# Optimization experiments

Measured on AMD Instinct MI355X. Metric: run time of the kernel, lower is better.

The kernel has to match this reference:

```python
import jax, jax.numpy as jnp
import numpy as np
from jax import lax

CHUNK = 64
EPS = 1e-5


def chunk_gla(q, k, v, g, chunk=CHUNK):
    """Gated linear attention, chunked parallel form (scale=1, as in HGRN2).
    q,k,g: [B,H,L,DK]; v: [B,H,L,DV]; g is per-step log decay on key dims.
    Recurrence: S_t = diag(exp(g_t)) S_{t-1} + k_t^T v_t ; o_t = q_t S_t.
    """
    B, H, L, DK = q.shape
    DV = v.shape[-1]
    n = L // chunk
    qc = q.reshape(B, H, n, chunk, DK)
    kc = k.reshape(B, H, n, chunk, DK)
    vc = v.reshape(B, H, n, chunk, DV)
    gc = jnp.cumsum(g.reshape(B, H, n, chunk, DK), axis=3)   # inclusive cumsum of log decays
    g_last = gc[..., -1:, :]                                 # [B,H,n,1,DK] total chunk decay

    qg = qc * jnp.exp(gc)                 # decay-weighted queries
    kg = kc * jnp.exp(g_last - gc)        # keys scaled to end-of-chunk
    kd = kc * jnp.exp(-gc)                # keys unscaled for intra-chunk attn

    # intra-chunk causal attention
    A = jnp.einsum('bhntd,bhnsd->bhnts', qg, kd)
    mask = jnp.tril(jnp.ones((chunk, chunk), dtype=bool))
    A = jnp.where(mask, A, 0.0)
    o_intra = jnp.einsum('bhnts,bhnsd->bhntd', A, vc)

    # inter-chunk recurrence over n chunks
    def step(S, inp):
        qg_c, kg_c, vc_c, gl_c = inp  # [B,H,C,DK], [B,H,C,DK], [B,H,C,DV], [B,H,DK]
        o = jnp.einsum('bhtd,bhdv->bhtv', qg_c, S)
        S = S * jnp.exp(gl_c)[..., None] + jnp.einsum('bhtd,bhtv->bhdv', kg_c, vc_c)
        return S, o

    S0 = jnp.zeros((B, H, DK, DV), q.dtype)
    xs = (jnp.moveaxis(qg, 2, 0), jnp.moveaxis(kg, 2, 0),
          jnp.moveaxis(vc, 2, 0), jnp.moveaxis(g_last[..., 0, :], 2, 0))
    _, o_inter = lax.scan(step, S0, xs)   # [n,B,H,C,DV]
    o = o_intra + jnp.moveaxis(o_inter, 0, 2)
    return o.reshape(B, H, L, DV)


def rms_norm(x, w, eps=EPS):
    var = jnp.mean(jnp.square(x), axis=-1, keepdims=True)
    return x * lax.rsqrt(var + eps) * w


def setup_inputs() -> dict:
    key = jax.random.key(0)
    B, L, D = 4, 2048, 2048
    ks = jax.random.split(key, 6)
    s = 1.0 / np.sqrt(D)
    return {
        'x': jax.random.normal(ks[0], (B, L, D), jnp.float32),
        'Wq': jax.random.normal(ks[1], (D, D), jnp.float32) * s,
        'Wf': jax.random.normal(ks[2], (D, D), jnp.float32) * s,
        'Wi': jax.random.normal(ks[3], (D, D), jnp.float32) * s,
        'Wo': jax.random.normal(ks[4], (D, D), jnp.float32) * s,
        'gnorm_w': jnp.ones((D,), jnp.float32),
    }


def reference(x, Wq, Wf, Wi, Wo, gnorm_w):
    B, L, D = x.shape
    H = 16
    Dh = D // H

    q = jax.nn.sigmoid(x @ Wq.T)
    f = jax.nn.sigmoid(x @ Wf.T)
    i = x @ Wi.T
    k = 1.0 - f
    g = jnp.log(f)

    def split_heads(t):  # b l (h d) -> b h l d
        return t.reshape(B, L, H, Dh).transpose(0, 2, 1, 3)

    q, k, i, g = map(split_heads, (q, k, i, g))
    o = chunk_gla(q, k, i, g)                  # [B,H,L,Dh]
    o = o.transpose(0, 2, 1, 3).reshape(B, L, D)
    o = rms_norm(o, gnorm_w)
    return o @ Wo.T
```

## Files before the change

kernel.cpp:

```cpp
#include <hip/hip_runtime.h>
#include <math.h>

typedef __bf16 bf16_t;
typedef __bf16 bf16x8 __attribute__((ext_vector_type(8)));
typedef float  f32x4  __attribute__((ext_vector_type(4)));

__device__ __forceinline__ void gl2lds16(const void* g, void* l) {
  __builtin_amdgcn_global_load_lds((__attribute__((address_space(1))) void*)g,
                                   (__attribute__((address_space(3))) void*)l,
                                   16, 0, 0);
}

#define MFMA16(a, b, c) __builtin_amdgcn_mfma_f32_16x16x32_bf16(a, b, c, 0, 0, 0)

template<int MODE>
__global__ __launch_bounds__(256, 2)
void gemm_bt2(const bf16_t* __restrict__ A, const bf16_t* __restrict__ Bw,
              bf16_t* __restrict__ oq, bf16_t* __restrict__ okk,
              bf16_t* __restrict__ ov, float* __restrict__ og,
              float* __restrict__ of, const float* __restrict__ rsc,
              int M, int N, int K)
{
  __shared__ __align__(16) bf16_t As[128 * 64];
  __shared__ __align__(16) bf16_t Bs[128 * 64];
  const int tt   = threadIdx.x;
  const int wave = tt >> 6;
  const int lane = tt & 63;
  const int nbn = N >> 7;
  const int m0 = (int)(blockIdx.x / nbn) << 7;
  const int n0 = (int)(blockIdx.x % nbn) << 7;
  const int wr = (wave >> 1) * 64;
  const int wc = (wave & 1) * 64;
  const int l15 = lane & 15, lq = lane >> 4;

  const int tk0 = (lq * 16) ^ ((lane & 7) << 4);
  const int tk1 = (64 + lq * 16) ^ ((lane & 7) << 4);

  const int srow = wave * 8 + (lane >> 3);
  const int sg = (lane & 7) ^ (lane >> 3);
  const bf16_t* pA = A  + (size_t)(m0 + srow) * K + sg * 8;
  const bf16_t* pB = Bw + (size_t)(n0 + srow) * K + sg * 8;

  f32x4 acc[4][4] = {};

  for (int kt = 0; kt < K; kt += 64) {
    #pragma unroll
    for (int i = 0; i < 4; i++) {
      gl2lds16(pA + (size_t)i * 32 * K + kt, (void*)(As + wave * 512 + i * 2048));
      gl2lds16(pB + (size_t)i * 32 * K + kt, (void*)(Bs + wave * 512 + i * 2048));
    }
    asm volatile("s_waitcnt vmcnt(0)" ::: "memory");
    __syncthreads();

    bf16x8 a[2][4], b[2][4];
    #pragma unroll
    for (int mf = 0; mf < 4; mf++) {
      const char* rp = (const char*)As + (wr + mf * 16 + l15) * 128;
      a[0][mf] = *(const bf16x8*)(rp + tk0);
      a[1][mf] = *(const bf16x8*)(rp + tk1);
    }
    #pragma unroll
    for (int nf = 0; nf < 4; nf++) {
      const char* rp = (const char*)Bs + (wc + nf * 16 + l15) * 128;
      b[0][nf] = *(const bf16x8*)(rp + tk0);
      b[1][nf] = *(const bf16x8*)(rp + tk1);
    }
    #pragma unroll
    for (int kh = 0; kh < 2; kh++)
      #pragma unroll
      for (int mf = 0; mf < 4; mf++)
        #pragma unroll
        for (int nf = 0; nf < 4; nf++)
          acc[mf][nf] = MFMA16(a[kh][mf], b[kh][nf], acc[mf][nf]);
    __syncthreads();
  }

  const int er = lq * 4;
  if (MODE == 0) {
    const int seg = n0 >> 11;
    const int gc = (n0 & 2047) + wc;
    #pragma unroll
    for (int mf = 0; mf < 4; mf++)
      #pragma unroll
      for (int nf = 0; nf < 4; nf++) {
        const int gr = m0 + wr + mf * 16 + er;
        #pragma unroll
        for (int jj = 0; jj < 4; jj++) {
          const size_t off2 = (size_t)(gr + jj) * 2048 + gc + nf * 16 + l15;
          const float v = acc[mf][nf][jj];
          if (seg == 0) {
            oq[off2] = (bf16_t)(1.0f / (1.0f + expf(-v)));
          } else if (seg == 1) {
            okk[off2] = (bf16_t)(1.0f / (1.0f + expf(v)));
            og[off2] = fminf(v, 0.0f) - log1pf(expf(-fabsf(v)));
          } else {
            ov[off2] = (bf16_t)v;
          }
        }
      }
  } else {
    const int gc = n0 + wc + l15;
    #pragma unroll
    for (int mf = 0; mf < 4; mf++) {
      const int gr = m0 + wr + mf * 16 + er;
      #pragma unroll
      for (int jj = 0; jj < 4; jj++) {
        const float s = rsc[gr + jj];
        #pragma unroll
        for (int nf = 0; nf < 4; nf++)
          of[(size_t)(gr + jj) * N + gc + nf * 16] = acc[mf][nf][jj] * s;
      }
    }
  }
}

__global__ void f2b_kernel(const float* __restrict__ in, bf16_t* __restrict__ out, int n8)
{
  const int idx = blockIdx.x * 256 + threadIdx.x;
  if (idx >= n8) return;
  const float4 a = *(const float4*)(in + (size_t)idx * 8);
  const float4 b = *(const float4*)(in + (size_t)idx * 8 + 4);
  bf16x8 o;
  o[0] = (bf16_t)a.x; o[1] = (bf16_t)a.y; o[2] = (bf16_t)a.z; o[3] = (bf16_t)a.w;
  o[4] = (bf16_t)b.x; o[5] = (bf16_t)b.y; o[6] = (bf16_t)b.z; o[7] = (bf16_t)b.w;
  *(bf16x8*)(out + (size_t)idx * 8) = o;
}

__global__ void f2b3_kernel(const float* __restrict__ w0, const float* __restrict__ w1,
                            const float* __restrict__ w2, bf16_t* __restrict__ out, int n8)
{
  const int idx = blockIdx.x * 256 + threadIdx.x;
  if (idx >= 3 * n8) return;
  const int which = idx / n8, j = idx - which * n8;
  const float* src = (which == 0) ? w0 : (which == 1) ? w1 : w2;
  const float4 a = *(const float4*)(src + (size_t)j * 8);
  const float4 b = *(const float4*)(src + (size_t)j * 8 + 4);
  bf16x8 o;
  o[0] = (bf16_t)a.x; o[1] = (bf16_t)a.y; o[2] = (bf16_t)a.z; o[3] = (bf16_t)a.w;
  o[4] = (bf16_t)b.x; o[5] = (bf16_t)b.y; o[6] = (bf16_t)b.z; o[7] = (bf16_t)b.w;
  *(bf16x8*)(out + (size_t)idx * 8) = o;
}

__global__ void f2bw_kernel(const float* __restrict__ in, const float* __restrict__ gw,
                            bf16_t* __restrict__ out, int n8)
{
  const int idx = blockIdx.x * 256 + threadIdx.x;
  if (idx >= n8) return;
  const int k0 = (idx * 8) & 2047;
  const float4 a = *(const float4*)(in + (size_t)idx * 8);
  const float4 b = *(const float4*)(in + (size_t)idx * 8 + 4);
  const float4 g0 = *(const float4*)(gw + k0);
  const float4 g1 = *(const float4*)(gw + k0 + 4);
  bf16x8 o;
  o[0] = (bf16_t)(a.x * g0.x); o[1] = (bf16_t)(a.y * g0.y);
  o[2] = (bf16_t)(a.z * g0.z); o[3] = (bf16_t)(a.w * g0.w);
  o[4] = (bf16_t)(b.x * g1.x); o[5] = (bf16_t)(b.y * g1.y);
  o[6] = (bf16_t)(b.z * g1.z); o[7] = (bf16_t)(b.w * g1.w);
  *(bf16x8*)(out + (size_t)idx * 8) = o;
}

__global__ __launch_bounds__(256)
void prep2_kernel(bf16_t* __restrict__ qb, bf16_t* __restrict__ kb,
                  const float* __restrict__ g32, float* __restrict__ eglh)
{
  __shared__ __align__(16) float gs[64][132];
  __shared__ float gls[128];
  const int blk = blockIdx.x;
  const int c = blk & 31, h = (blk >> 5) & 15, b = blk >> 9;
  const size_t row0 = (size_t)b * 2048 + (size_t)c * 64;
  const int col0 = h * 128;
  const int tt = threadIdx.x;

  #pragma unroll
  for (int s = 0; s < 8; s++) {
    const int u = tt + s * 256;
    const int t = u >> 5, d4 = (u & 31) * 4;
    *(float4*)&gs[t][d4] = *(const float4*)(g32 + (row0 + t) * 2048 + col0 + d4);
  }
  __syncthreads();
  if (tt < 128) {
    float run = 0.0f;
    for (int t = 0; t < 64; t++) { run += gs[t][tt]; gs[t][tt] = run; }
    gls[tt] = 0.5f * run;
    eglh[(size_t)blk * 128 + tt] = expf(0.5f * run);
  }
  __syncthreads();
  #pragma unroll
  for (int s = 0; s < 4; s++) {
    const int u = tt + s * 256;
    const int t = u >> 4, d8 = (u & 15) * 8;
    bf16_t* qp = qb + (row0 + t) * 2048 + col0 + d8;
    bf16_t* kp = kb + (row0 + t) * 2048 + col0 + d8;
    const bf16x8 q8 = *(const bf16x8*)qp;
    const bf16x8 k8 = *(const bf16x8*)kp;
    bf16x8 qo, ko2;
    #pragma unroll
    for (int j = 0; j < 8; j++) {
      const float gc = gs[t][d8 + j];
      const float gh = gls[d8 + j];
      qo[j]  = (bf16_t)((float)q8[j] * expf(gc - gh));
      ko2[j] = (bf16_t)((float)k8[j] * expf(gh - gc));
    }
    *(bf16x8*)qp = qo;
    *(bf16x8*)kp = ko2;
  }
}

__global__ __launch_bounds__(256)
void state2_kernel(const bf16_t* __restrict__ kb, const bf16_t* __restrict__ vb,
                   const float* __restrict__ eglh, bf16_t* __restrict__ ST)
{
  __shared__ __align__(16) bf16_t kgt[64][72];
  __shared__ __align__(16) bf16_t vt[64][72];
  __shared__ float ehs[64];
  const int blk = blockIdx.x;
  const int dh = blk & 1, eh = (blk >> 1) & 1, bh = blk >> 2;
  const int b = bh >> 4, h = bh & 15;
  const int col0 = h * 128;
  const int tt = threadIdx.x, wave = tt >> 6, lane = tt & 63;
  const int r = lane & 15, ko = (lane >> 4) * 8;
  const int d0 = dh * 64, e0 = eh * 64;
  f32x4 acc[4] = {};

  for (int c = 0; c < 32; c++) {
    const size_t cb = (size_t)bh * 32 + c;
    const size_t row0 = (size_t)b * 2048 + (size_t)c * 64;
    if (tt < 64) ehs[tt] = eglh[cb * 128 + d0 + tt];
    __syncthreads();
    #pragma unroll
    for (int s = 0; s < 2; s++) {
      const int u = tt + s * 256;
      const int t = u >> 3, d8 = (u & 7) * 8;
      const bf16x8 kv = *(const bf16x8*)(kb + (row0 + t) * 2048 + col0 + d0 + d8);
      const bf16x8 vv = *(const bf16x8*)(vb + (row0 + t) * 2048 + col0 + e0 + d8);
      #pragma unroll
      for (int j = 0; j < 8; j++) {
        kgt[d8 + j][t] = (bf16_t)((float)kv[j] * ehs[d8 + j]);
        vt[d8 + j][t]  = vv[j];
      }
    }
    __syncthreads();
    #pragma unroll
    for (int nf = 0; nf < 4; nf++) {
      const int d = nf * 16 + r;
      const float sd = ehs[d];
      #pragma unroll
      for (int jj = 0; jj < 4; jj++) {
        const int e = e0 + wave * 16 + (lane >> 4) * 4 + jj;
        ST[(cb * 128 + e) * 128 + d0 + d] = (bf16_t)(acc[nf][jj] * sd);
      }
    }
    #pragma unroll
    for (int nf = 0; nf < 4; nf++) {
      const float ev = ehs[nf * 16 + r];
      const float e2 = ev * ev;
      #pragma unroll
      for (int jj = 0; jj < 4; jj++) acc[nf][jj] *= e2;
    }
    #pragma unroll
    for (int ks = 0; ks < 2; ks++) {
      const bf16x8 a = *(const bf16x8*)&vt[wave * 16 + r][ks * 32 + ko];
      #pragma unroll
      for (int nf = 0; nf < 4; nf++) {
        const bf16x8 bfr = *(const bf16x8*)&kgt[nf * 16 + r][ks * 32 + ko];
        acc[nf] = MFMA16(a, bfr, acc[nf]);
      }
    }
    __syncthreads();
  }
}

__global__ __launch_bounds__(256)
void chunk2_kernel(const bf16_t* __restrict__ qb, const bf16_t* __restrict__ kb,
                   const bf16_t* __restrict__ vb, const bf16_t* __restrict__ ST,
                   bf16_t* __restrict__ o16)
{
  __shared__ __align__(16) bf16_t qgs[64][136];
  __shared__ __align__(16) bf16_t kds[64][136];
  __shared__ __align__(16) bf16_t vTs[128][72];
  __shared__ __align__(16) bf16_t Ps[64][72];
  const int blk = blockIdx.x;
  const int c = blk & 31, h = (blk >> 5) & 15, b = blk >> 9;
  const size_t row0 = (size_t)b * 2048 + (size_t)c * 64;
  const int col0 = h * 128;
  const int tt = threadIdx.x, wave = tt >> 6, lane = tt & 63;
  const int r = lane & 15, ko = (lane >> 4) * 8;

  #pragma unroll
  for (int s = 0; s < 4; s++) {
    const int u = tt + s * 256;
    const int t = u >> 4, d8 = (u & 15) * 8;
    *(bf16x8*)&qgs[t][d8] = *(const bf16x8*)(qb + (row0 + t) * 2048 + col0 + d8);
    *(bf16x8*)&kds[t][d8] = *(const bf16x8*)(kb + (row0 + t) * 2048 + col0 + d8);
  }
  #pragma unroll
  for (int s = 0; s < 4; s++) {
    const int u = tt + s * 256;
    const int t = u >> 4, e8 = (u & 15) * 8;
    const bf16x8 vv = *(const bf16x8*)(vb + (row0 + t) * 2048 + col0 + e8);
    #pragma unroll
    for (int j = 0; j < 8; j++) vTs[e8 + j][t] = vv[j];
  }
  __syncthreads();

  bf16x8 aq[4];
  #pragma unroll
  for (int ks = 0; ks < 4; ks++) aq[ks] = *(const bf16x8*)&qgs[wave * 16 + r][ks * 32 + ko];

  f32x4 accA[4] = {};
  #pragma unroll
  for (int ks = 0; ks < 4; ks++)
    #pragma unroll
    for (int sf = 0; sf < 4; sf++) {
      const bf16x8 bfr = *(const bf16x8*)&kds[sf * 16 + r][ks * 32 + ko];
      accA[sf] = MFMA16(aq[ks], bfr, accA[sf]);
    }

  #pragma unroll
  for (int sf = 0; sf < 4; sf++)
    #pragma unroll
    for (int jj = 0; jj < 4; jj++) {
      const int t = wave * 16 + (lane >> 4) * 4 + jj;
      const int s = sf * 16 + r;
      Ps[t][s] = (bf16_t)(t >= s ? accA[sf][jj] : 0.0f);
    }

  f32x4 acc[8] = {};
  const size_t stbase = (size_t)blk * 128 * 128;
  #pragma unroll
  for (int ks = 0; ks < 4; ks++)
    #pragma unroll
    for (int ne = 0; ne < 8; ne++) {
      const bf16x8 bfr = *(const bf16x8*)(ST + stbase + (size_t)(ne * 16 + r) * 128 + ks * 32 + ko);
      acc[ne] = MFMA16(aq[ks], bfr, acc[ne]);
    }
  #pragma unroll
  for (int ks = 0; ks < 2; ks++) {
    const bf16x8 pa = *(const bf16x8*)&Ps[wave * 16 + r][ks * 32 + ko];
    #pragma unroll
    for (int ne = 0; ne < 8; ne++) {
      const bf16x8 bfr = *(const bf16x8*)&vTs[ne * 16 + r][ks * 32 + ko];
      acc[ne] = MFMA16(pa, bfr, acc[ne]);
    }
  }

  #pragma unroll
  for (int ne = 0; ne < 8; ne++)
    #pragma unroll
    for (int jj = 0; jj < 4; jj++) {
      const int t = wave * 16 + (lane >> 4) * 4 + jj;
      const int e = ne * 16 + r;
      o16[(row0 + t) * 2048 + col0 + e] = (bf16_t)acc[ne][jj];
    }
}

__global__ __launch_bounds__(256)
void rmsr_kernel(const bf16_t* __restrict__ o16, float* __restrict__ rsc)
{
  __shared__ float red[4];
  const size_t row = blockIdx.x;
  const int tt = threadIdx.x;
  const bf16x8 v = *(const bf16x8*)(o16 + row * 2048 + tt * 8);
  float ss = 0.0f;
  #pragma unroll
  for (int j = 0; j < 8; j++) { const float f = (float)v[j]; ss += f * f; }
  #pragma unroll
  for (int off = 32; off > 0; off >>= 1) ss += __shfl_down(ss, off);
  if ((tt & 63) == 0) red[tt >> 6] = ss;
  __syncthreads();
  if (tt == 0)
    rsc[row] = rsqrtf((red[0] + red[1] + red[2] + red[3]) * (1.0f / 2048.0f) + 1e-5f);
}

extern "C" void kernel_launch(void* const* d_in, const int* in_sizes, int n_in,
                              void* d_out, int out_size, void* d_ws, size_t ws_size,
                              hipStream_t stream)
{
  const float* x  = (const float*)d_in[0];
  const float* Wq = (const float*)d_in[1];
  const float* Wf = (const float*)d_in[2];
  const float* Wi = (const float*)d_in[3];
  const float* Wo = (const float*)d_in[4];
  const float* gw = (const float*)d_in[5];
  float* out = (float*)d_out;
  char* ws = (char*)d_ws;

  const int K = 2048;
  const size_t MB = 1ull << 20;

  auto run = [&](const float* xs, float* outs, int nbs) {
    const int Ms = nbs * 2048;
    const size_t Sx = (size_t)Ms * 2048 * 2;
    bf16_t* xb  = (bf16_t*)(ws + 0);
    bf16_t* qb  = (bf16_t*)(ws + Sx);
    bf16_t* kb  = (bf16_t*)(ws + 2 * Sx);
    bf16_t* vb  = (bf16_t*)(ws + 3 * Sx);
    float*  g32 = (float*) (ws + 4 * Sx);
    bf16_t* Wb  = (bf16_t*)(ws + 6 * Sx);
    float*  egh = (float*) (ws + 6 * Sx + 24 * MB);
    float*  rsc = (float*) (ws + 6 * Sx + 25 * MB);
    bf16_t* STp = (bf16_t*)(ws + 4 * Sx);
    bf16_t* o16 = (bf16_t*)(ws + 0);

    const int n8x = Ms * 2048 / 8;
    const int n8w = 2048 * 2048 / 8;

    f2b_kernel<<<(n8x + 255) / 256, 256, 0, stream>>>(xs, xb, n8x);
    f2b3_kernel<<<(3 * n8w + 255) / 256, 256, 0, stream>>>(Wq, Wf, Wi, Wb, n8w);

    gemm_bt2<0><<<(Ms / 128) * (6144 / 128), 256, 0, stream>>>(
        xb, Wb, qb, kb, vb, g32, nullptr, nullptr, Ms, 6144, K);

    prep2_kernel<<<nbs * 512, 256, 0, stream>>>(qb, kb, g32, egh);
    state2_kernel<<<nbs * 64, 256, 0, stream>>>(kb, vb, egh, STp);
    chunk2_kernel<<<nbs * 512, 256, 0, stream>>>(qb, kb, vb, STp, o16);
    rmsr_kernel<<<Ms, 256, 0, stream>>>(o16, rsc);

    f2bw_kernel<<<(n8w + 255) / 256, 256, 0, stream>>>(Wo, gw, Wb, n8w);
    gemm_bt2<1><<<(Ms / 128) * (2048 / 128), 256, 0, stream>>>(
        o16, Wb, nullptr, nullptr, nullptr, nullptr, outs, rsc, Ms, 2048, K);
  };

  const size_t Sx_full = (size_t)8192 * 2048 * 2;
  const size_t need_full = 6 * Sx_full + 26 * MB;
  if (ws_size >= need_full) {
    run(x, out, 4);
  } else {
    for (int sb = 0; sb < 4; sb++)
      run(x + (size_t)sb * 2048 * 2048, out + (size_t)sb * 2048 * 2048, 1);
  }

  (void)in_sizes; (void)n_in; (void)out_size;
}
```

Baseline: 591.0 us.

## Use 256x256 double-buffered LDS GEMM for fused QKV projection

Replaces the 128x128 tile GEMM for the QKV projection (M=8192, N=6144) with a new 512-thread kernel using 256x256 tiles. Each k-step is staged into a second 64KB LDS buffer with async global-to-LDS loads while the current one is computed, so loads overlap with MFMA work. Larger tiles raise arithmetic intensity and cut global traffic. In exchange, 128KB of dynamic LDS and 128 accumulator registers per lane limit occupancy to one block per CU, and the grid shrinks to 768 blocks. The output projection keeps the old kernel, now specialised to that single mode.

```diff
diff --git a/kernel.cpp b/kernel.cpp
--- a/kernel.cpp
+++ b/kernel.cpp
@@ -13,11 +13,106 @@
 
 #define MFMA16(a, b, c) __builtin_amdgcn_mfma_f32_16x16x32_bf16(a, b, c, 0, 0, 0)
 
-template<int MODE>
+__global__ __launch_bounds__(512, 1)
+void gemm256s(const bf16_t* __restrict__ A, const bf16_t* __restrict__ Bw,
+              bf16_t* __restrict__ oq, bf16_t* __restrict__ okk,
+              bf16_t* __restrict__ ov, float* __restrict__ og,
+              int M, int N, int K)
+{
+  extern __shared__ __align__(16) char smem[];
+  const int tt = threadIdx.x;
+  const int wave = tt >> 6, lane = tt & 63;
+  const int wm = wave >> 2, wn = wave & 3;
+  const int nbn = N >> 8;
+  const int m0 = (int)(blockIdx.x / nbn) << 8;
+  const int n0 = (int)(blockIdx.x % nbn) << 8;
+  const int l15 = lane & 15, lq = lane >> 4;
+
+  const int tk0 = (lq * 16) ^ ((lane & 7) << 4);
+  const int tk1 = (64 + lq * 16) ^ ((lane & 7) << 4);
+
+  const int srow = tt >> 3;
+  const int sg = (tt & 7) ^ (srow & 7);
+  const bf16_t* pA = A  + (size_t)(m0 + srow) * K + sg * 8;
+  const bf16_t* pB = Bw + (size_t)(n0 + srow) * K + sg * 8;
+  const size_t rstep = (size_t)64 * K;
+
+  f32x4 acc[8][4] = {};
+  const int T = K >> 6;
+
+  auto stage = [&](int t, int sl) {
+    const int kt = t << 6;
+    char* base = smem + sl * 65536 + tt * 16;
+    #pragma unroll
+    for (int i = 0; i < 4; i++) {
+      gl2lds16(pA + i * rstep + kt, base + i * 8192);
+      gl2lds16(pB + i * rstep + kt, base + 32768 + i * 8192);
+    }
+  };
+
+  stage(0, 0);
+
+  for (int t = 0; t < T; t++) {
+    const int s = t & 1;
+    asm volatile("s_waitcnt vmcnt(0)" ::: "memory");
+    __builtin_amdgcn_s_barrier();
+    if (t + 1 < T) stage(t + 1, s ^ 1);
+
+    const char* as = smem + s * 65536;
+    const char* bs = as + 32768;
+
+    bf16x8 bfr[4][2];
+    #pragma unroll
+    for (int nf = 0; nf < 4; nf++) {
+      const char* rp = bs + (wn * 64 + nf * 16 + l15) * 128;
+      bfr[nf][0] = *(const bf16x8*)(rp + tk0);
+      bfr[nf][1] = *(const bf16x8*)(rp + tk1);
+    }
+    #pragma unroll
+    for (int h = 0; h < 2; h++) {
+      bf16x8 af[4][2];
+      #pragma unroll
+      for (int mf = 0; mf < 4; mf++) {
+        const char* rp = as + (wm * 128 + (h * 4 + mf) * 16 + l15) * 128;
+        af[mf][0] = *(const bf16x8*)(rp + tk0);
+        af[mf][1] = *(const bf16x8*)(rp + tk1);
+      }
+      #pragma unroll
+      for (int mf = 0; mf < 4; mf++)
+        #pragma unroll
+        for (int nf = 0; nf < 4; nf++) {
+          acc[h * 4 + mf][nf] = MFMA16(af[mf][0], bfr[nf][0], acc[h * 4 + mf][nf]);
+          acc[h * 4 + mf][nf] = MFMA16(af[mf][1], bfr[nf][1], acc[h * 4 + mf][nf]);
+        }
+    }
+  }
+
+  const int er = lq * 4;
+  const int seg = n0 >> 11;
+  const int gc = (n0 & 2047) + wn * 64 + l15;
+  #pragma unroll
+  for (int mf = 0; mf < 8; mf++)
+    #pragma unroll
+    for (int nf = 0; nf < 4; nf++) {
+      const int gr = m0 + wm * 128 + mf * 16 + er;
+      #pragma unroll
+      for (int jj = 0; jj < 4; jj++) {
+        const size_t off2 = (size_t)(gr + jj) * 2048 + gc + nf * 16;
+        const float v = acc[mf][nf][jj];
+        if (seg == 0) {
+          oq[off2] = (bf16_t)(1.0f / (1.0f + expf(-v)));
+        } else if (seg == 1) {
+          okk[off2] = (bf16_t)(1.0f / (1.0f + expf(v)));
+          og[off2] = fminf(v, 0.0f) - log1pf(expf(-fabsf(v)));
+        } else {
+          ov[off2] = (bf16_t)v;
+        }
+      }
+    }
+}
+
 __global__ __launch_bounds__(256, 2)
 void gemm_bt2(const bf16_t* __restrict__ A, const bf16_t* __restrict__ Bw,
-              bf16_t* __restrict__ oq, bf16_t* __restrict__ okk,
-              bf16_t* __restrict__ ov, float* __restrict__ og,
               float* __restrict__ of, const float* __restrict__ rsc,
               int M, int N, int K)
 {
@@ -76,40 +171,16 @@
   }
 
   const int er = lq * 4;
-  if (MODE == 0) {
-    const int seg = n0 >> 11;
-    const int gc = (n0 & 2047) + wc;
-    #pragma unroll
-    for (int mf = 0; mf < 4; mf++)
-      #pragma unroll
-      for (int nf = 0; nf < 4; nf++) {
-        const int gr = m0 + wr + mf * 16 + er;
-        #pragma unroll
-        for (int jj = 0; jj < 4; jj++) {
-          const size_t off2 = (size_t)(gr + jj) * 2048 + gc + nf * 16 + l15;
-          const float v = acc[mf][nf][jj];
-          if (seg == 0) {
-            oq[off2] = (bf16_t)(1.0f / (1.0f + expf(-v)));
-          } else if (seg == 1) {
-            okk[off2] = (bf16_t)(1.0f / (1.0f + expf(v)));
-            og[off2] = fminf(v, 0.0f) - log1pf(expf(-fabsf(v)));
-          } else {
-            ov[off2] = (bf16_t)v;
-          }
-        }
-      }
-  } else {
-    const int gc = n0 + wc + l15;
-    #pragma unroll
-    for (int mf = 0; mf < 4; mf++) {
-      const int gr = m0 + wr + mf * 16 + er;
-      #pragma unroll
-      for (int jj = 0; jj < 4; jj++) {
-        const float s = rsc[gr + jj];
-        #pragma unroll
-        for (int nf = 0; nf < 4; nf++)
-          of[(size_t)(gr + jj) * N + gc + nf * 16] = acc[mf][nf][jj] * s;
-      }
+  const int gc = n0 + wc + l15;
+  #pragma unroll
+  for (int mf = 0; mf < 4; mf++) {
+    const int gr = m0 + wr + mf * 16 + er;
+    #pragma unroll
+    for (int jj = 0; jj < 4; jj++) {
+      const float s = rsc[gr + jj];
+      #pragma unroll
+      for (int nf = 0; nf < 4; nf++)
+        of[(size_t)(gr + jj) * N + gc + nf * 16] = acc[mf][nf][jj] * s;
     }
   }
 }
@@ -387,6 +458,10 @@
 
   const int K = 2048;
   const size_t MB = 1ull << 20;
+  const int LDS = 131072;
+
+  (void)hipFuncSetAttribute((const void*)gemm256s,
+      hipFuncAttributeMaxDynamicSharedMemorySize, LDS);
 
   auto run = [&](const float* xs, float* outs, int nbs) {
     const int Ms = nbs * 2048;
@@ -408,8 +483,8 @@
     f2b_kernel<<<(n8x + 255) / 256, 256, 0, stream>>>(xs, xb, n8x);
     f2b3_kernel<<<(3 * n8w + 255) / 256, 256, 0, stream>>>(Wq, Wf, Wi, Wb, n8w);
 
-    gemm_bt2<0><<<(Ms / 128) * (6144 / 128), 256, 0, stream>>>(
-        xb, Wb, qb, kb, vb, g32, nullptr, nullptr, Ms, 6144, K);
+    gemm256s<<<(Ms / 256) * (6144 / 256), 512, LDS, stream>>>(
+        xb, Wb, qb, kb, vb, g32, Ms, 6144, K);
 
     prep2_kernel<<<nbs * 512, 256, 0, stream>>>(qb, kb, g32, egh);
     state2_kernel<<<nbs * 64, 256, 0, stream>>>(kb, vb, egh, STp);
@@ -417,8 +492,8 @@
     rmsr_kernel<<<Ms, 256, 0, stream>>>(o16, rsc);
 
     f2bw_kernel<<<(n8w + 255) / 256, 256, 0, stream>>>(Wo, gw, Wb, n8w);
-    gemm_bt2<1><<<(Ms / 128) * (2048 / 128), 256, 0, stream>>>(
-        o16, Wb, nullptr, nullptr, nullptr, nullptr, outs, rsc, Ms, 2048, K);
+    gemm_bt2<<<(Ms / 128) * (2048 / 128), 256, 0, stream>>>(
+        o16, Wb, outs, rsc, Ms, 2048, K);
   };
 
   const size_t Sx_full = (size_t)8192 * 2048 * 2;
```

Measured after the change: 826.1 us. +39.8%, slower.
